# Kernel tuning notes

Measured on AMD Instinct MI355X. Metric: run time of the kernel, lower is better.

## Reference

```python
import jax, jax.numpy as jnp
import numpy as np

N_HEADS = 16
D_MODEL = 1024


def setup_inputs() -> dict:
    key = jax.random.key(0)
    ks = jax.random.split(key, 9)
    B, S, D = 2, 2048, D_MODEL
    scale = 1.0 / np.sqrt(D)
    inp = {
        "x": jax.random.normal(ks[0], (B, S, D), dtype=jnp.float32),
        "wq": jax.random.normal(ks[1], (D, D), dtype=jnp.float32) * scale,
        "bq": jax.random.normal(ks[2], (D,), dtype=jnp.float32) * 0.01,
        "wk": jax.random.normal(ks[3], (D, D), dtype=jnp.float32) * scale,
        "bk": jax.random.normal(ks[4], (D,), dtype=jnp.float32) * 0.01,
        "wv": jax.random.normal(ks[5], (D, D), dtype=jnp.float32) * scale,
        "bv": jax.random.normal(ks[6], (D,), dtype=jnp.float32) * 0.01,
        "wo": jax.random.normal(ks[7], (D, D), dtype=jnp.float32) * scale,
        "bo": jax.random.normal(ks[8], (D,), dtype=jnp.float32) * 0.01,
    }
    return inp


def reference(x, wq, bq, wk, bk, wv, bv, wo, bo):
    B, S, D = x.shape
    H = N_HEADS
    hd = D // H
    # projections -> [B, H, S, hd]
    def proj(w, b):
        return (x @ w + b).reshape(B, S, H, hd).transpose(0, 2, 1, 3)
    q = proj(wq, bq)
    k = proj(wk, bk)
    v = proj(wv, bv)
    scores = jnp.einsum("bhqd,bhkd->bhqk", q, k) * (1.0 / np.sqrt(hd))
    # causal mask: future tokens (col > row) -> -inf
    causal = jnp.tril(jnp.ones((S, S), dtype=bool))  # True = allowed
    scores = jnp.where(causal[None, None, :, :], scores, -jnp.inf)
    att = jax.nn.softmax(scores, axis=-1)
    y = jnp.einsum("bhqk,bhkd->bhqd", att, v)  # [B,H,S,hd]
    y = y.transpose(0, 2, 1, 3).reshape(B, S, D)
    return y @ wo + bo
```

## Files before the change

### kernel.cpp

```cpp
#include <hip/hip_runtime.h>
#include <hip/hip_bf16.h>
#include <math.h>

typedef unsigned short u16;
typedef __bf16 bf16x8 __attribute__((ext_vector_type(8)));
typedef short s16x4 __attribute__((ext_vector_type(4)));
typedef float f32x4 __attribute__((ext_vector_type(4)));
typedef u16 u16x8 __attribute__((ext_vector_type(8)));
typedef u16 u16x4 __attribute__((ext_vector_type(4)));

#define DM 1024
#define NH 16
#define SL 2048
#define BB 2
#define TOK (BB * SL)

__device__ __forceinline__ u16 f2bf(float f) {
  union { float f; unsigned u; } v; v.f = f;
  unsigned r = v.u + 0x7FFFu + ((v.u >> 16) & 1u);
  return (u16)(r >> 16);
}

__device__ __forceinline__ float fexp2(float x) {
  float r; asm("v_exp_f32 %0, %1" : "=v"(r) : "v"(x)); return r;
}

__device__ __forceinline__ unsigned cvtpk(float lo, float hi) {
  unsigned r;
  asm("v_cvt_pk_bf16_f32 %0, %1, %2" : "=v"(r) : "v"(lo), "v"(hi));
  return r;
}

__device__ __forceinline__ f32x4 pv_mfma(s16x4 a, s16x4 b, f32x4 c) {
#if __has_builtin(__builtin_amdgcn_mfma_f32_16x16x16bf16_1k)
  return __builtin_amdgcn_mfma_f32_16x16x16bf16_1k(a, b, c, 0, 0, 0);
#else
  asm("v_mfma_f32_16x16x16_bf16 %0, %1, %2, %0" : "+v"(c) : "v"(a), "v"(b));
  return c;
#endif
}

typedef __attribute__((address_space(1))) const unsigned GU;
typedef __attribute__((address_space(3))) unsigned LU;
#define GLOAD16(g, l) __builtin_amdgcn_global_load_lds((GU*)(g), (LU*)(l), 16, 0, 0)

__global__ void cast_bf16(const float* __restrict__ in, u16* __restrict__ out, int n) {
  int i = (blockIdx.x * blockDim.x + threadIdx.x) * 8;
  if (i + 8 <= n) {
    float4 a = *(const float4*)(in + i);
    float4 b = *(const float4*)(in + i + 4);
    u16x8 o;
    o[0]=f2bf(a.x); o[1]=f2bf(a.y); o[2]=f2bf(a.z); o[3]=f2bf(a.w);
    o[4]=f2bf(b.x); o[5]=f2bf(b.y); o[6]=f2bf(b.z); o[7]=f2bf(b.w);
    *(u16x8*)(out + i) = o;
  }
}

__global__ __launch_bounds__(256) void transpose_cast4(
    const float* __restrict__ w0, const float* __restrict__ w1,
    const float* __restrict__ w2, const float* __restrict__ w3,
    u16* __restrict__ out) {
  __shared__ u16 T[64][72];
  int mat = blockIdx.z;
  const float* in = (mat == 0) ? w0 : (mat == 1) ? w1 : (mat == 2) ? w2 : w3;
  u16* o = out + ((size_t)mat << 20);
  int k0 = blockIdx.x * 64, n0 = blockIdx.y * 64;
  int tid = threadIdx.x;
  int r = tid >> 2;
  int c0 = (tid & 3) * 16;
#pragma unroll
  for (int j = 0; j < 16; j += 4) {
    float4 f = *(const float4*)(in + (size_t)(k0 + r) * 1024 + n0 + c0 + j);
    T[c0 + j + 0][r] = f2bf(f.x);
    T[c0 + j + 1][r] = f2bf(f.y);
    T[c0 + j + 2][r] = f2bf(f.z);
    T[c0 + j + 3][r] = f2bf(f.w);
  }
  __syncthreads();
  int n = tid >> 2, k1 = (tid & 3) * 16;
#pragma unroll
  for (int j = 0; j < 16; j += 8)
    *(u16x8*)(o + (size_t)(n0 + n) * 1024 + k0 + k1 + j) = *(const u16x8*)&T[n][k1 + j];
}

template<int MODE>
__global__ __launch_bounds__(256) void gemm_qkv(
    const u16* __restrict__ A, const u16* __restrict__ Bt,
    const float* __restrict__ b0, const float* __restrict__ b1,
    const float* __restrict__ b2,
    u16* __restrict__ Qo, u16* __restrict__ Ko, u16* __restrict__ Vto,
    float* __restrict__ Fo)
{
  __shared__ u16 As[3][128 * 32];
  __shared__ u16 Bs[3][128 * 32];
  const int tid = threadIdx.x, lane = tid & 63, w = tid >> 6;
  const int fr = lane & 15, fq = lane >> 4;
  const int wr = w >> 1, wc = w & 1;
  const int m0 = blockIdx.x * 128;
  const int n0 = blockIdx.y * 128;
  f32x4 acc[4][4] = {};

  auto stage = [&](int buf, int k0) {
#pragma unroll
    for (int i = 0; i < 2; ++i) {
      int b16 = i * 256 + tid;
      int row = b16 >> 2, ch = b16 & 3;
      GLOAD16(A + (size_t)(m0 + row) * DM + k0 + ((ch ^ (row & 3)) * 8), &As[buf][b16 * 8]);
    }
#pragma unroll
    for (int i = 0; i < 2; ++i) {
      int b16 = i * 256 + tid;
      int row = b16 >> 2, ch = b16 & 3;
      GLOAD16(Bt + (size_t)(n0 + row) * DM + k0 + ((ch ^ (row & 3)) * 8), &Bs[buf][b16 * 8]);
    }
  };

  const int NK = DM / 32;
  stage(0, 0);
  stage(1, 32);
  for (int j = 0; j < NK; ++j) {
    if (j + 1 < NK) asm volatile("s_waitcnt vmcnt(4)" ::: "memory");
    else            asm volatile("s_waitcnt vmcnt(0)" ::: "memory");
    __builtin_amdgcn_s_barrier();
    __builtin_amdgcn_sched_barrier(0);

    const u16* Al = As[j % 3];
    const u16* Bl = Bs[j % 3];
    bf16x8 av[4], bv[4];
#pragma unroll
    for (int m = 0; m < 4; ++m) {
      int row = wr * 64 + m * 16 + fr;
      av[m] = *(const bf16x8*)&Al[row * 32 + ((fq ^ (row & 3)) * 8)];
    }
#pragma unroll
    for (int n = 0; n < 4; ++n) {
      int row = wc * 64 + n * 16 + fr;
      bv[n] = *(const bf16x8*)&Bl[row * 32 + ((fq ^ (row & 3)) * 8)];
    }
    __builtin_amdgcn_s_setprio(1);
#pragma unroll
    for (int m = 0; m < 4; ++m)
#pragma unroll
      for (int n = 0; n < 4; ++n)
        acc[m][n] = __builtin_amdgcn_mfma_f32_16x16x32_bf16(av[m], bv[n], acc[m][n], 0, 0, 0);
    __builtin_amdgcn_s_setprio(0);

    if (j + 2 < NK) stage((j + 2) % 3, (j + 2) * 32);
  }

  if (MODE == 0) {
    int nloc = n0 & 1023;
    int mat = n0 >> 10;
    const float* bias = (mat == 0) ? b0 : ((mat == 1) ? b1 : b2);
    const float scl = (mat == 0) ? 0.18033688f : 1.0f;
#pragma unroll
    for (int m = 0; m < 4; ++m) {
      int row = m0 + wr * 64 + m * 16 + fq * 4;
#pragma unroll
      for (int n = 0; n < 4; ++n) {
        int col = nloc + wc * 64 + n * 16 + fr;
        float bc = bias[col];
        if (mat == 2) {
          u16x4 v4;
#pragma unroll
          for (int r = 0; r < 4; ++r) v4[r] = f2bf(acc[m][n][r] + bc);
          *(u16x4*)(Vto + (size_t)col * TOK + row) = v4;
        } else {
          u16* dst = (mat == 0) ? Qo : Ko;
#pragma unroll
          for (int r = 0; r < 4; ++r)
            dst[(size_t)(row + r) * DM + col] = f2bf((acc[m][n][r] + bc) * scl);
        }
      }
    }
  } else {
#pragma unroll
    for (int m = 0; m < 4; ++m) {
      int row = m0 + wr * 64 + m * 16 + fq * 4;
#pragma unroll
      for (int n = 0; n < 4; ++n) {
        int col = n0 + wc * 64 + n * 16 + fr;
        float bc = b0[col];
#pragma unroll
        for (int r = 0; r < 4; ++r)
          Fo[(size_t)(row + r) * DM + col] = acc[m][n][r] + bc;
      }
    }
  }
}

__global__ __launch_bounds__(256, 4) void attn_kernel(
    const u16* __restrict__ Qg, const u16* __restrict__ Kg,
    const u16* __restrict__ Vt, u16* __restrict__ Og)
{
  __shared__ u16 SM[16384];
  const int tid = threadIdx.x, lane = tid & 63, w = tid >> 6;
  const int fr = lane & 15, fq = lane >> 4;
  const int bid = blockIdx.x;
  const int xcd = bid & 7;
  const int l = bid >> 3;
  const int bh = xcd * 4 + (l & 3);
  const int qt = 31 - (l >> 2);
  const int b = bh >> 4, h = bh & 15;
  const size_t rowbase = (size_t)b * SL;
  const int nt = qt + 1;

  const int qrow = qt * 64 + w * 16 + fr;
  bf16x8 qa[2];
#pragma unroll
  for (int c = 0; c < 2; ++c)
    qa[c] = *(const bf16x8*)(Qg + (rowbase + qrow) * DM + h * 64 + c * 32 + fq * 8);

  float mrow = -INFINITY, lsum = 0.f;
  f32x4 o[4] = {};

  auto stage = [&](int buf, int t) {
#pragma unroll
    for (int i = 0; i < 2; ++i) {
      int b16 = i * 256 + tid;
      int row = b16 >> 3, ch = b16 & 7;
      GLOAD16(Kg + (rowbase + t * 64 + row) * DM + h * 64 + ((ch ^ (row & 7)) * 8),
              &SM[buf * 4096 + b16 * 8]);
    }
#pragma unroll
    for (int i = 0; i < 2; ++i) {
      int b16 = i * 256 + tid;
      int row = b16 >> 3, ch = b16 & 7;
      GLOAD16(Vt + (size_t)(h * 64 + row) * TOK + b * SL + t * 64 + ((ch ^ (row & 7)) * 8),
              &SM[8192 + buf * 4096 + b16 * 8]);
    }
  };

  stage(0, 0);
  __syncthreads();
  int buf = 0;

  for (int t = 0; t < nt; ++t) {
    if (t + 1 < nt) stage(buf ^ 1, t + 1);
    const u16* Kl = &SM[buf * 4096];
    const u16* Vl = &SM[8192 + buf * 4096];

    f32x4 st[4];
    __builtin_amdgcn_s_setprio(1);
#pragma unroll
    for (int kb = 0; kb < 4; ++kb) {
      int row = kb * 16 + fr;
      bf16x8 kf0 = *(const bf16x8*)&Kl[row * 64 + ((fq ^ (row & 7)) * 8)];
      bf16x8 kf1 = *(const bf16x8*)&Kl[row * 64 + (((4 + fq) ^ (row & 7)) * 8)];
      f32x4 s0 = {};
      s0 = __builtin_amdgcn_mfma_f32_16x16x32_bf16(kf0, qa[0], s0, 0, 0, 0);
      st[kb] = __builtin_amdgcn_mfma_f32_16x16x32_bf16(kf1, qa[1], s0, 0, 0, 0);
    }
    __builtin_amdgcn_s_setprio(0);

    if (t == qt) {
      const int kvb = t * 64 + fq * 4;
#pragma unroll
      for (int kb = 0; kb < 4; ++kb)
#pragma unroll
        for (int r = 0; r < 4; ++r)
          if (kvb + kb * 16 + r > qrow) st[kb][r] = -INFINITY;
    }

    float pm = st[0][0];
#pragma unroll
    for (int kb = 0; kb < 4; ++kb)
#pragma unroll
      for (int r = 0; r < 4; ++r) pm = fmaxf(pm, st[kb][r]);
    pm = fmaxf(pm, __shfl_xor(pm, 16, 64));
    pm = fmaxf(pm, __shfl_xor(pm, 32, 64));

    if (__any(pm > mrow + 8.f)) {
      float nm = fmaxf(mrow, pm);
      float alpha = fexp2(mrow - nm);
      mrow = nm;
      lsum *= alpha;
#pragma unroll
      for (int db = 0; db < 4; ++db)
#pragma unroll
        for (int r = 0; r < 4; ++r) o[db][r] *= alpha;
    }

    unsigned pk2[4][2];
    float ps = 0.f;
#pragma unroll
    for (int kb = 0; kb < 4; ++kb) {
      float p0 = fexp2(st[kb][0] - mrow);
      float p1 = fexp2(st[kb][1] - mrow);
      float p2 = fexp2(st[kb][2] - mrow);
      float p3 = fexp2(st[kb][3] - mrow);
      ps += (p0 + p1) + (p2 + p3);
      pk2[kb][0] = cvtpk(p0, p1);
      pk2[kb][1] = cvtpk(p2, p3);
    }
    lsum += ps;

    __builtin_amdgcn_s_setprio(1);
#pragma unroll
    for (int kb = 0; kb < 4; ++kb) {
      union { unsigned u[2]; s16x4 s; } bb;
      bb.u[0] = pk2[kb][0]; bb.u[1] = pk2[kb][1];
#pragma unroll
      for (int db = 0; db < 4; ++db) {
        int row = db * 16 + fr;
        s16x4 vfr = *(const s16x4*)&Vl[row * 64 + (((kb * 2 + (fq >> 1)) ^ (row & 7)) * 8) + ((fq & 1) * 4)];
        o[db] = pv_mfma(vfr, bb.s, o[db]);
      }
    }
    __builtin_amdgcn_s_setprio(0);

    __syncthreads();
    buf ^= 1;
  }

  float L = lsum;
  L += __shfl_xor(L, 16, 64);
  L += __shfl_xor(L, 32, 64);
  float inv = 1.0f / L;

  u16* Tb = &SM[w * 1152];
#pragma unroll
  for (int db = 0; db < 4; ++db)
#pragma unroll
    for (int w2 = 0; w2 < 2; ++w2) {
      unsigned pk = cvtpk(o[db][2 * w2] * inv, o[db][2 * w2 + 1] * inv);
      *(unsigned*)&Tb[fr * 72 + db * 16 + fq * 4 + 2 * w2] = pk;
    }
  int rr = lane >> 2, cc = (lane & 3) * 16;
  size_t gbase = (rowbase + qt * 64 + w * 16 + rr) * DM + h * 64 + cc;
#pragma unroll
  for (int j = 0; j < 2; ++j)
    *(u16x8*)(Og + gbase + j * 8) = *(const u16x8*)&Tb[rr * 72 + cc + j * 8];
}

extern "C" void kernel_launch(void* const* d_in, const int* in_sizes, int n_in,
                              void* d_out, int out_size, void* d_ws, size_t ws_size,
                              hipStream_t stream) {
  const float* x  = (const float*)d_in[0];
  const float* wq = (const float*)d_in[1];
  const float* bq = (const float*)d_in[2];
  const float* wk = (const float*)d_in[3];
  const float* bk = (const float*)d_in[4];
  const float* wv = (const float*)d_in[5];
  const float* bv = (const float*)d_in[6];
  const float* wo = (const float*)d_in[7];
  const float* bo = (const float*)d_in[8];

  char* ws = (char*)d_ws;
  u16* Xb   = (u16*)ws;
  u16* Wall = (u16*)(ws + 8u  * 1024 * 1024);
  u16* Qb   = (u16*)(ws + 16u * 1024 * 1024);
  u16* Kb   = (u16*)(ws + 24u * 1024 * 1024);
  u16* VtG  = (u16*)(ws + 32u * 1024 * 1024);

  const int nX = TOK * DM;
  hipLaunchKernelGGL(cast_bf16, dim3(nX / (256 * 8)), dim3(256), 0, stream, x, Xb, nX);
  hipLaunchKernelGGL(transpose_cast4, dim3(16, 16, 4), dim3(256), 0, stream, wq, wk, wv, wo, Wall);

  hipLaunchKernelGGL((gemm_qkv<0>), dim3(TOK / 128, 3072 / 128), dim3(256), 0, stream,
                     Xb, Wall, bq, bk, bv, Qb, Kb, VtG, (float*)nullptr);

  hipLaunchKernelGGL(attn_kernel, dim3(32 * BB * NH), dim3(256), 0, stream,
                     Qb, Kb, VtG, Xb);

  hipLaunchKernelGGL((gemm_qkv<1>), dim3(TOK / 128, DM / 128), dim3(256), 0, stream,
                     Xb, Wall + 3u * (1u << 20), bo, (const float*)nullptr, (const float*)nullptr,
                     (u16*)nullptr, (u16*)nullptr, (u16*)nullptr, (float*)d_out);
}
```

Measured before the change: 108.6 us.

## Process 128 query rows per attention block, two 16-row tiles per wave

The attention kernel now gives each block 128 query rows instead of 64, with each wave handling two 16-row query sub-tiles that share every K/V fragment loaded from LDS. This halves the grid and halves the K/V global and LDS traffic per query row, at the cost of more registers per thread (doubled accumulators and softmax state) and fewer blocks to balance the causal workload. Masking now applies on the last two KV tiles of each block, and the epilogue writes 32 rows per wave.

```diff
diff --git a/kernel.cpp b/kernel.cpp
--- a/kernel.cpp
+++ b/kernel.cpp
@@ -200,19 +200,23 @@
   const int xcd = bid & 7;
   const int l = bid >> 3;
   const int bh = xcd * 4 + (l & 3);
-  const int qt = 31 - (l >> 2);
+  const int qt = 15 - (l >> 2);
   const int b = bh >> 4, h = bh & 15;
   const size_t rowbase = (size_t)b * SL;
-  const int nt = qt + 1;
-
-  const int qrow = qt * 64 + w * 16 + fr;
-  bf16x8 qa[2];
-#pragma unroll
-  for (int c = 0; c < 2; ++c)
-    qa[c] = *(const bf16x8*)(Qg + (rowbase + qrow) * DM + h * 64 + c * 32 + fq * 8);
-
-  float mrow = -INFINITY, lsum = 0.f;
-  f32x4 o[4] = {};
+  const int nt = 2 * qt + 2;
+
+  bf16x8 qa[2][2];
+#pragma unroll
+  for (int mr = 0; mr < 2; ++mr) {
+    int qrow = qt * 128 + w * 32 + mr * 16 + fr;
+#pragma unroll
+    for (int c = 0; c < 2; ++c)
+      qa[mr][c] = *(const bf16x8*)(Qg + (rowbase + qrow) * DM + h * 64 + c * 32 + fq * 8);
+  }
+
+  float mrow[2] = { -INFINITY, -INFINITY };
+  float lsum[2] = { 0.f, 0.f };
+  f32x4 o[2][4] = {};
 
   auto stage = [&](int buf, int t) {
 #pragma unroll
@@ -240,71 +244,81 @@
     const u16* Kl = &SM[buf * 4096];
     const u16* Vl = &SM[8192 + buf * 4096];
 
-    f32x4 st[4];
+    f32x4 st[2][4];
     __builtin_amdgcn_s_setprio(1);
 #pragma unroll
     for (int kb = 0; kb < 4; ++kb) {
       int row = kb * 16 + fr;
       bf16x8 kf0 = *(const bf16x8*)&Kl[row * 64 + ((fq ^ (row & 7)) * 8)];
       bf16x8 kf1 = *(const bf16x8*)&Kl[row * 64 + (((4 + fq) ^ (row & 7)) * 8)];
-      f32x4 s0 = {};
-      s0 = __builtin_amdgcn_mfma_f32_16x16x32_bf16(kf0, qa[0], s0, 0, 0, 0);
-      st[kb] = __builtin_amdgcn_mfma_f32_16x16x32_bf16(kf1, qa[1], s0, 0, 0, 0);
+#pragma unroll
+      for (int mr = 0; mr < 2; ++mr) {
+        f32x4 s0 = {};
+        s0 = __builtin_amdgcn_mfma_f32_16x16x32_bf16(kf0, qa[mr][0], s0, 0, 0, 0);
+        st[mr][kb] = __builtin_amdgcn_mfma_f32_16x16x32_bf16(kf1, qa[mr][1], s0, 0, 0, 0);
+      }
     }
     __builtin_amdgcn_s_setprio(0);
 
-    if (t == qt) {
-      const int kvb = t * 64 + fq * 4;
+    const bool maskt = (t >= 2 * qt);
+    unsigned pk2[2][4][2];
+#pragma unroll
+    for (int mr = 0; mr < 2; ++mr) {
+      if (maskt) {
+        const int qrow = qt * 128 + w * 32 + mr * 16 + fr;
+        const int kvb = t * 64 + fq * 4;
+#pragma unroll
+        for (int kb = 0; kb < 4; ++kb)
+#pragma unroll
+          for (int r = 0; r < 4; ++r)
+            if (kvb + kb * 16 + r > qrow) st[mr][kb][r] = -INFINITY;
+      }
+      float pm = st[mr][0][0];
 #pragma unroll
       for (int kb = 0; kb < 4; ++kb)
 #pragma unroll
-        for (int r = 0; r < 4; ++r)
-          if (kvb + kb * 16 + r > qrow) st[kb][r] = -INFINITY;
-    }
-
-    float pm = st[0][0];
-#pragma unroll
-    for (int kb = 0; kb < 4; ++kb)
-#pragma unroll
-      for (int r = 0; r < 4; ++r) pm = fmaxf(pm, st[kb][r]);
-    pm = fmaxf(pm, __shfl_xor(pm, 16, 64));
-    pm = fmaxf(pm, __shfl_xor(pm, 32, 64));
-
-    if (__any(pm > mrow + 8.f)) {
-      float nm = fmaxf(mrow, pm);
-      float alpha = fexp2(mrow - nm);
-      mrow = nm;
-      lsum *= alpha;
-#pragma unroll
-      for (int db = 0; db < 4; ++db)
-#pragma unroll
-        for (int r = 0; r < 4; ++r) o[db][r] *= alpha;
-    }
-
-    unsigned pk2[4][2];
-    float ps = 0.f;
+        for (int r = 0; r < 4; ++r) pm = fmaxf(pm, st[mr][kb][r]);
+      pm = fmaxf(pm, __shfl_xor(pm, 16, 64));
+      pm = fmaxf(pm, __shfl_xor(pm, 32, 64));
+
+      if (__any(pm > mrow[mr] + 8.f)) {
+        float nm = fmaxf(mrow[mr], pm);
+        float alpha = fexp2(mrow[mr] - nm);
+        mrow[mr] = nm;
+        lsum[mr] *= alpha;
+#pragma unroll
+        for (int db = 0; db < 4; ++db)
+#pragma unroll
+          for (int r = 0; r < 4; ++r) o[mr][db][r] *= alpha;
+      }
+
+      float ps = 0.f;
+#pragma unroll
+      for (int kb = 0; kb < 4; ++kb) {
+        float p0 = fexp2(st[mr][kb][0] - mrow[mr]);
+        float p1 = fexp2(st[mr][kb][1] - mrow[mr]);
+        float p2 = fexp2(st[mr][kb][2] - mrow[mr]);
+        float p3 = fexp2(st[mr][kb][3] - mrow[mr]);
+        ps += (p0 + p1) + (p2 + p3);
+        pk2[mr][kb][0] = cvtpk(p0, p1);
+        pk2[mr][kb][1] = cvtpk(p2, p3);
+      }
+      lsum[mr] += ps;
+    }
+
+    __builtin_amdgcn_s_setprio(1);
 #pragma unroll
     for (int kb = 0; kb < 4; ++kb) {
-      float p0 = fexp2(st[kb][0] - mrow);
-      float p1 = fexp2(st[kb][1] - mrow);
-      float p2 = fexp2(st[kb][2] - mrow);
-      float p3 = fexp2(st[kb][3] - mrow);
-      ps += (p0 + p1) + (p2 + p3);
-      pk2[kb][0] = cvtpk(p0, p1);
-      pk2[kb][1] = cvtpk(p2, p3);
-    }
-    lsum += ps;
-
-    __builtin_amdgcn_s_setprio(1);
-#pragma unroll
-    for (int kb = 0; kb < 4; ++kb) {
-      union { unsigned u[2]; s16x4 s; } bb;
-      bb.u[0] = pk2[kb][0]; bb.u[1] = pk2[kb][1];
 #pragma unroll
       for (int db = 0; db < 4; ++db) {
         int row = db * 16 + fr;
         s16x4 vfr = *(const s16x4*)&Vl[row * 64 + (((kb * 2 + (fq >> 1)) ^ (row & 7)) * 8) + ((fq & 1) * 4)];
-        o[db] = pv_mfma(vfr, bb.s, o[db]);
+#pragma unroll
+        for (int mr = 0; mr < 2; ++mr) {
+          union { unsigned u[2]; s16x4 s; } bb;
+          bb.u[0] = pk2[mr][kb][0]; bb.u[1] = pk2[mr][kb][1];
+          o[mr][db] = pv_mfma(vfr, bb.s, o[mr][db]);
+        }
       }
     }
     __builtin_amdgcn_s_setprio(0);
@@ -313,24 +327,29 @@
     buf ^= 1;
   }
 
-  float L = lsum;
-  L += __shfl_xor(L, 16, 64);
-  L += __shfl_xor(L, 32, 64);
-  float inv = 1.0f / L;
-
-  u16* Tb = &SM[w * 1152];
-#pragma unroll
-  for (int db = 0; db < 4; ++db)
-#pragma unroll
-    for (int w2 = 0; w2 < 2; ++w2) {
-      unsigned pk = cvtpk(o[db][2 * w2] * inv, o[db][2 * w2 + 1] * inv);
-      *(unsigned*)&Tb[fr * 72 + db * 16 + fq * 4 + 2 * w2] = pk;
-    }
-  int rr = lane >> 2, cc = (lane & 3) * 16;
-  size_t gbase = (rowbase + qt * 64 + w * 16 + rr) * DM + h * 64 + cc;
-#pragma unroll
-  for (int j = 0; j < 2; ++j)
-    *(u16x8*)(Og + gbase + j * 8) = *(const u16x8*)&Tb[rr * 72 + cc + j * 8];
+  float inv[2];
+#pragma unroll
+  for (int mr = 0; mr < 2; ++mr) {
+    float L = lsum[mr];
+    L += __shfl_xor(L, 16, 64);
+    L += __shfl_xor(L, 32, 64);
+    inv[mr] = 1.0f / L;
+  }
+  u16* Tb = &SM[w * 2304];
+#pragma unroll
+  for (int mr = 0; mr < 2; ++mr)
+#pragma unroll
+    for (int db = 0; db < 4; ++db)
+#pragma unroll
+      for (int w2 = 0; w2 < 2; ++w2) {
+        unsigned pk = cvtpk(o[mr][db][2 * w2] * inv[mr], o[mr][db][2 * w2 + 1] * inv[mr]);
+        *(unsigned*)&Tb[(mr * 16 + fr) * 72 + db * 16 + fq * 4 + 2 * w2] = pk;
+      }
+  int rr = lane >> 1, cc = (lane & 1) * 32;
+  size_t gbase = (rowbase + qt * 128 + w * 32 + rr) * DM + h * 64 + cc;
+#pragma unroll
+  for (int i = 0; i < 4; ++i)
+    *(u16x8*)(Og + gbase + i * 8) = *(const u16x8*)&Tb[rr * 72 + cc + i * 8];
 }
 
 extern "C" void kernel_launch(void* const* d_in, const int* in_sizes, int n_in,
@@ -360,7 +379,7 @@
   hipLaunchKernelGGL((gemm_qkv<0>), dim3(TOK / 128, 3072 / 128), dim3(256), 0, stream,
                      Xb, Wall, bq, bk, bv, Qb, Kb, VtG, (float*)nullptr);
 
-  hipLaunchKernelGGL(attn_kernel, dim3(32 * BB * NH), dim3(256), 0, stream,
+  hipLaunchKernelGGL(attn_kernel, dim3(16 * BB * NH), dim3(256), 0, stream,
                      Qb, Kb, VtG, Xb);
 
   hipLaunchKernelGGL((gemm_qkv<1>), dim3(TOK / 128, DM / 128), dim3(256), 0, stream,
```

After: 118.0 us. 1.09x slower.
